# Optimization experiments

Measured on AMD Instinct MI355X. Metric: run time of the kernel, lower is better.

Reference implementation:

```python
import jax, jax.numpy as jnp
import numpy as np

N = 50000   # nodes
E = 800000  # edges
F_IN, H, C, G = 128, 96, 16, 128  # features, hidden, classes, graphs


def gelu(x):
    return jax.nn.gelu(x, approximate=False)  # torch F.gelu default (erf)


def gcn_conv(x, W, b, src, dst, dis):
    # PyG GCNConv improved=True: A_hat = A + 2I, out = D^-1/2 A_hat D^-1/2 (x W) + b
    xw = x @ W                                   # [N, out]
    norm = dis[src] * dis[dst]                   # [E]
    msg = norm[:, None] * xw[src]                # gather + scale
    out = jax.ops.segment_sum(msg, dst, num_segments=N)
    out = out + (2.0 * dis * dis)[:, None] * xw  # self-loop with weight 2
    return out + b


def setup_inputs() -> dict:
    key = jax.random.key(0)
    ks = jax.random.split(key, 12)
    x = jax.random.normal(ks[0], (N, F_IN), dtype=jnp.float32)
    edge_index = jax.random.randint(ks[1], (2, E), 0, N, dtype=jnp.int64)
    batch = jnp.sort(jax.random.randint(ks[2], (N,), 0, G, dtype=jnp.int64))
    s = lambda fan_in: 1.0 / np.sqrt(fan_in)
    W0 = jax.random.uniform(ks[3], (F_IN, H), jnp.float32, -s(F_IN), s(F_IN))
    b0 = jnp.zeros((H,), jnp.float32)
    W1 = jax.random.uniform(ks[4], (H, H), jnp.float32, -s(H), s(H))
    b1 = jnp.zeros((H,), jnp.float32)
    W2 = jax.random.uniform(ks[5], (H, H), jnp.float32, -s(H), s(H))
    b2 = jnp.zeros((H,), jnp.float32)
    Wc1 = jax.random.uniform(ks[6], (2 * H, H), jnp.float32, -s(2 * H), s(2 * H))
    bc1 = jax.random.uniform(ks[7], (H,), jnp.float32, -s(2 * H), s(2 * H))
    Wc2 = jax.random.uniform(ks[8], (H, C), jnp.float32, -s(H), s(H))
    bc2 = jax.random.uniform(ks[9], (C,), jnp.float32, -s(H), s(H))
    return {"x": x, "edge_index": edge_index, "batch": batch,
            "W0": W0, "b0": b0, "W1": W1, "b1": b1, "W2": W2, "b2": b2,
            "Wc1": Wc1, "bc1": bc1, "Wc2": Wc2, "bc2": bc2}


def reference(x, edge_index, batch, W0, b0, W1, b1, W2, b2, Wc1, bc1, Wc2, bc2):
    src, dst = edge_index[0], edge_index[1]
    # degrees including self-loop weight 2 (improved=True)
    deg = jax.ops.segment_sum(jnp.ones((E,), x.dtype), dst, num_segments=N) + 2.0
    dis = jax.lax.rsqrt(deg)
    # layer 0: GCNConv(F_IN -> H)
    h = gcn_conv(x, W0, b0, src, dst, dis)
    # residual GCNConv layers (dropout is identity at inference)
    h = h + gcn_conv(gelu(h), W1, b1, src, dst, dis)
    h = h + gcn_conv(gelu(h), W2, b2, src, dst, dis)
    h = gelu(h)
    # global mean + max pooling per graph
    cnt = jax.ops.segment_sum(jnp.ones((N,), h.dtype), batch, num_segments=G)
    mean_p = jax.ops.segment_sum(h, batch, num_segments=G) / cnt[:, None]
    max_p = jax.ops.segment_max(h, batch, num_segments=G)
    p = jnp.concatenate([mean_p, max_p], axis=1)  # [G, 2H]
    p = p @ Wc1 + bc1
    p = gelu(p)
    return p @ Wc2 + bc2
```

## Files before the change

### kernel.cpp

```cpp
#include <hip/hip_runtime.h>
#include <hip/hip_bf16.h>

#define DEVINL __device__ __forceinline__

constexpr int N = 50000;
constexpr int E = 800000;
constexpr int F_IN = 128;
constexpr int H = 96;
constexpr int C = 16;
constexpr int G = 128;
constexpr int S = 8;
constexpr int ELLW = 64;

constexpr int OFF_W0  = 0;
constexpr int OFF_W1  = OFF_W0 + F_IN * H;
constexpr int OFF_W2  = OFF_W1 + H * H;
constexpr int OFF_WC1 = OFF_W2 + H * H;
constexpr int OFF_WC2 = OFF_WC1 + 2 * H * H;
constexpr int OFF_B0  = OFF_WC2 + H * C;
constexpr int OFF_B1  = OFF_B0 + H;
constexpr int OFF_B2  = OFF_B1 + H;
constexpr int OFF_BC1 = OFF_B2 + H;
constexpr int OFF_BC2 = OFF_BC1 + H;
constexpr int WF_TOT  = OFF_BC2 + C;

constexpr int CVB   = (WF_TOT + 255) / 256;
constexpr int GEMB  = (N + 31) / 32;
constexpr int SCATB = (E / 2 + 127) / 128;

DEVINL float gelu_f(float x) {
    return 0.5f * x * (1.0f + erff(x * 0.70710678118654752440f));
}

DEVINL int detect_eidx_i64(const int* e) {
    int z = 0;
#pragma unroll
    for (int i = 1; i < 16; i += 2) z |= e[i];
    return z == 0;
}
DEVINL int detect_batch_i64(const int* a) {
    int z = 0;
    for (int i = 20001; i < 20032; i += 2) z |= a[i];
    return z == 0;
}
DEVINL int detect_x_f32(const unsigned short* xu) {
    int bad = 0;
    for (int i = 0; i < 128; i += 2) { int ex = (xu[i] >> 7) & 0xFF; if (ex >= 132) bad = 1; }
    return bad;
}

DEVINL unsigned pk(float a, float b) {
    __hip_bfloat16 ha = __float2bfloat16(a), hb = __float2bfloat16(b);
    unsigned short ua = *(unsigned short*)&ha, ub = *(unsigned short*)&hb;
    return (unsigned)ua | ((unsigned)ub << 16);
}
DEVINL float lo16(unsigned u) { return __uint_as_float(u << 16); }
DEVINL float hi16(unsigned u) { return __uint_as_float(u & 0xffff0000u); }

DEVINL float disv(int c) { return rsqrtf((float)c + 2.0f); }

__global__ void k_prep(const void* W0, const void* W1, const void* W2,
                       const void* Wc1, const void* Wc2,
                       const void* b0, const void* b1, const void* b2,
                       const void* bc1, const void* bc2,
                       const void* x, float* __restrict__ wf, int* __restrict__ cnt) {
    int i = blockIdx.x * 256 + threadIdx.x;
    if (i < N) cnt[i] = 0;
    if (i >= WF_TOT) return;
    int f32 = detect_x_f32((const unsigned short*)x);
    const void* src; int j;
    if      (i < OFF_W1)  { src = W0;  j = i - OFF_W0; }
    else if (i < OFF_W2)  { src = W1;  j = i - OFF_W1; }
    else if (i < OFF_WC1) { src = W2;  j = i - OFF_W2; }
    else if (i < OFF_WC2) { src = Wc1; j = i - OFF_WC1; }
    else if (i < OFF_B0)  { src = Wc2; j = i - OFF_WC2; }
    else if (i < OFF_B1)  { src = b0;  j = i - OFF_B0; }
    else if (i < OFF_B2)  { src = b1;  j = i - OFF_B1; }
    else if (i < OFF_BC1) { src = b2;  j = i - OFF_B2; }
    else if (i < OFF_BC2) { src = bc1; j = i - OFF_BC1; }
    else                  { src = bc2; j = i - OFF_BC2; }
    wf[i] = f32 ? ((const float*)src)[j]
                : __bfloat162float(((const __hip_bfloat16*)src)[j]);
}

template<int K, int KC, bool RAW_IN, bool GELU_IN, bool SCALE_OUT>
DEVINL void gemm_tile(const void* __restrict__ inp, const float* __restrict__ Wf,
                      const int* __restrict__ cnt,
                      int xf32, unsigned* __restrict__ out, int bid, int t) {
    constexpr int R = 32;
    constexpr int NC = K / KC;
    __shared__ __align__(16) float xs[KC][R + 4];
    __shared__ __align__(16) float wsh[KC * 96];
    const int r0 = bid * R;
    const int ty = t >> 4;
    const int tx = t & 15;

    float acc[4][6];
#pragma unroll
    for (int i = 0; i < 4; ++i)
#pragma unroll
        for (int j = 0; j < 6; ++j) acc[i][j] = 0.f;

    for (int c = 0; c < NC; ++c) {
        if (c) __syncthreads();
        for (int idx = t * 4; idx < KC * 96; idx += 128 * 4)
            *(float4*)&wsh[idx] = *(const float4*)&Wf[c * KC * 96 + idx];
        if (RAW_IN && !xf32) {
            for (int idx = t; idx < R * KC; idx += 128) {
                int r = idx / KC, kk = idx - r * KC;
                int row = r0 + r, k = c * KC + kk;
                float v = 0.f;
                if (row < N) v = __bfloat162float(((const __hip_bfloat16*)inp)[(size_t)row * K + k]);
                xs[kk][r] = v;
            }
        } else {
            constexpr int KC4 = KC / 4;
            for (int idx = t; idx < R * KC4; idx += 128) {
                int r = idx / KC4, k4 = (idx - r * KC4) * 4;
                int row = r0 + r, k = c * KC + k4;
                float4 v = make_float4(0.f, 0.f, 0.f, 0.f);
                if (row < N) v = *(const float4*)((const float*)inp + (size_t)row * K + k);
                if (GELU_IN) { v.x = gelu_f(v.x); v.y = gelu_f(v.y); v.z = gelu_f(v.z); v.w = gelu_f(v.w); }
                xs[k4 + 0][r] = v.x; xs[k4 + 1][r] = v.y; xs[k4 + 2][r] = v.z; xs[k4 + 3][r] = v.w;
            }
        }
        __syncthreads();

#pragma unroll 4
        for (int kk = 0; kk < KC; ++kk) {
            float4 av = *(const float4*)&xs[kk][ty * 4];
            float2 b0 = *(const float2*)&wsh[kk * 96 + tx * 6];
            float2 b1 = *(const float2*)&wsh[kk * 96 + tx * 6 + 2];
            float2 b2 = *(const float2*)&wsh[kk * 96 + tx * 6 + 4];
            float a[4] = {av.x, av.y, av.z, av.w};
            float b[6] = {b0.x, b0.y, b1.x, b1.y, b2.x, b2.y};
#pragma unroll
            for (int i = 0; i < 4; ++i)
#pragma unroll
                for (int j = 0; j < 6; ++j)
                    acc[i][j] = fmaf(a[i], b[j], acc[i][j]);
        }
    }

#pragma unroll
    for (int i = 0; i < 4; ++i) {
        int row = r0 + ty * 4 + i;
        if (row < N) {
            float d = SCALE_OUT ? disv(cnt[row]) : 1.0f;
            unsigned* o = out + (size_t)row * 48 + tx * 3;
            o[0] = pk(d * acc[i][0], d * acc[i][1]);
            o[1] = pk(d * acc[i][2], d * acc[i][3]);
            o[2] = pk(d * acc[i][4], d * acc[i][5]);
        }
    }
}

__global__ __launch_bounds__(128) void k_sg(const void* __restrict__ x,
                                            const float* __restrict__ Wf,
                                            const int* __restrict__ eidx,
                                            int* __restrict__ cnt, int* __restrict__ ell,
                                            unsigned* __restrict__ outZ) {
    int b = blockIdx.x, t = threadIdx.x;
    if (b % 3 == 0) {
        int gb = b / 3;
        if (gb >= GEMB) return;
        int xf32 = detect_x_f32((const unsigned short*)x);
        gemm_tile<F_IN, 32, true, false, false>(x, Wf, nullptr, xf32, outZ, gb, t);
        return;
    }
    int sb = (b / 3) * 2 + (b % 3) - 1;
    if (sb >= SCATB) return;
    int t2 = sb * 128 + t;
    int e = 2 * t2;
    if (e >= E) return;
    int i64 = detect_eidx_i64(eidx);
    int s0, s1, d0, d1;
    if (i64) {
        int4 sp = *(const int4*)(eidx + 4 * t2);
        int4 dp = *(const int4*)(eidx + 2 * E + 4 * t2);
        s0 = sp.x; s1 = sp.z; d0 = dp.x; d1 = dp.z;
    } else {
        int2 sp = *(const int2*)(eidx + 2 * t2);
        int2 dp = *(const int2*)(eidx + E + 2 * t2);
        s0 = sp.x; s1 = sp.y; d0 = dp.x; d1 = dp.y;
    }
    int p0 = atomicAdd(&cnt[d0], 1);
    if (p0 < ELLW) ell[d0 * ELLW + p0] = s0;
    if (e + 1 < E) {
        int p1 = atomicAdd(&cnt[d1], 1);
        if (p1 < ELLW) ell[d1 * ELLW + p1] = s1;
    }
}

template<int K, int KC, bool GELU_IN>
__global__ __launch_bounds__(128) void k_gemm(const float* __restrict__ inp,
                                              const float* __restrict__ Wf,
                                              const int* __restrict__ cnt,
                                              unsigned* __restrict__ out) {
    gemm_tile<K, KC, false, GELU_IN, true>(inp, Wf, cnt, 1, out, blockIdx.x, threadIdx.x);
}

template<bool PRESCALED>
__global__ __launch_bounds__(256) void k_aggr(const unsigned* __restrict__ xw, const float* res,
                                              const int* __restrict__ ell, const int* __restrict__ cnt,
                                              const float* __restrict__ bias, float* __restrict__ out) {
    __shared__ int   sIdx[4][ELLW];
    __shared__ float sW[4][ELLW];
    int wid = threadIdx.x >> 6, lane = threadIdx.x & 63;
    int n = blockIdx.x * 4 + wid;
    if (n >= N) return;
    int cn = cnt[n];
    int cc = min(cn, ELLW);
    if (lane < cc) {
        int idx = ell[n * ELLW + lane];
        sIdx[wid][lane] = idx;
        if (!PRESCALED) sW[wid][lane] = disv(cnt[idx]);
    }
    int slot = lane / 12;
    int li = lane - slot * 12;
    int cp = li * 4;

    int   idxs[5];
    float ws[5];
#pragma unroll
    for (int s = 0; s < 5; ++s) {
        int js = slot + 5 * s;
        bool valid = (slot < 5) && (js < cc);
        int raw = sIdx[wid][js & (ELLW - 1)];
        float rw = PRESCALED ? 1.f : sW[wid][js & (ELLW - 1)];
        idxs[s] = valid ? raw : n;
        ws[s]   = valid ? rw : 0.f;
    }
    uint4 u0 = *(const uint4*)(xw + (size_t)idxs[0] * 48 + cp);
    uint4 u1 = *(const uint4*)(xw + (size_t)idxs[1] * 48 + cp);
    uint4 u2 = *(const uint4*)(xw + (size_t)idxs[2] * 48 + cp);
    uint4 u3 = *(const uint4*)(xw + (size_t)idxs[3] * 48 + cp);
    uint4 u4 = *(const uint4*)(xw + (size_t)idxs[4] * 48 + cp);

    float4 A0 = make_float4(0.f, 0.f, 0.f, 0.f);
    float4 A1 = make_float4(0.f, 0.f, 0.f, 0.f);
#define ACCW(W_, U_) \
    A0.x = fmaf(W_, lo16((U_).x), A0.x); A0.y = fmaf(W_, hi16((U_).x), A0.y); \
    A0.z = fmaf(W_, lo16((U_).y), A0.z); A0.w = fmaf(W_, hi16((U_).y), A0.w); \
    A1.x = fmaf(W_, lo16((U_).z), A1.x); A1.y = fmaf(W_, hi16((U_).z), A1.y); \
    A1.z = fmaf(W_, lo16((U_).w), A1.z); A1.w = fmaf(W_, hi16((U_).w), A1.w);
    ACCW(ws[0], u0)
    ACCW(ws[1], u1)
    ACCW(ws[2], u2)
    ACCW(ws[3], u3)
    ACCW(ws[4], u4)

    int jt = (slot < 5) ? (25 + slot) : cc;
    for (; jt < cc; jt += 5) {
        int sdx = sIdx[wid][jt];
        uint4 u = *(const uint4*)(xw + (size_t)sdx * 48 + cp);
        float wt = PRESCALED ? 1.f : sW[wid][jt];
        ACCW(wt, u)
    }
#undef ACCW

    {
        float g0, g1, g2, g3;
        g0 = __shfl(A0.x, lane + 12); g1 = __shfl(A0.x, lane + 24); g2 = __shfl(A0.x, lane + 36); g3 = __shfl(A0.x, lane + 48);
        A0.x += g0 + g1 + g2 + g3;
        g0 = __shfl(A0.y, lane + 12); g1 = __shfl(A0.y, lane + 24); g2 = __shfl(A0.y, lane + 36); g3 = __shfl(A0.y, lane + 48);
        A0.y += g0 + g1 + g2 + g3;
        g0 = __shfl(A0.z, lane + 12); g1 = __shfl(A0.z, lane + 24); g2 = __shfl(A0.z, lane + 36); g3 = __shfl(A0.z, lane + 48);
        A0.z += g0 + g1 + g2 + g3;
        g0 = __shfl(A0.w, lane + 12); g1 = __shfl(A0.w, lane + 24); g2 = __shfl(A0.w, lane + 36); g3 = __shfl(A0.w, lane + 48);
        A0.w += g0 + g1 + g2 + g3;
        g0 = __shfl(A1.x, lane + 12); g1 = __shfl(A1.x, lane + 24); g2 = __shfl(A1.x, lane + 36); g3 = __shfl(A1.x, lane + 48);
        A1.x += g0 + g1 + g2 + g3;
        g0 = __shfl(A1.y, lane + 12); g1 = __shfl(A1.y, lane + 24); g2 = __shfl(A1.y, lane + 36); g3 = __shfl(A1.y, lane + 48);
        A1.y += g0 + g1 + g2 + g3;
        g0 = __shfl(A1.z, lane + 12); g1 = __shfl(A1.z, lane + 24); g2 = __shfl(A1.z, lane + 36); g3 = __shfl(A1.z, lane + 48);
        A1.z += g0 + g1 + g2 + g3;
        g0 = __shfl(A1.w, lane + 12); g1 = __shfl(A1.w, lane + 24); g2 = __shfl(A1.w, lane + 36); g3 = __shfl(A1.w, lane + 48);
        A1.w += g0 + g1 + g2 + g3;
    }

    if (lane < 12) {
        float dn = disv(cn);
        float sc = PRESCALED ? (2.f * dn) : (2.f * dn * dn);
        int cl = li * 8;
        uint4 su = *(const uint4*)(xw + (size_t)n * 48 + cp);
        float4 sv0 = make_float4(lo16(su.x), hi16(su.x), lo16(su.y), hi16(su.y));
        float4 sv1 = make_float4(lo16(su.z), hi16(su.z), lo16(su.w), hi16(su.w));
        float4 bv0 = *(const float4*)(bias + cl);
        float4 bv1 = *(const float4*)(bias + cl + 4);
        float4 rv0 = make_float4(0.f, 0.f, 0.f, 0.f);
        float4 rv1 = make_float4(0.f, 0.f, 0.f, 0.f);
        if (res) {
            rv0 = *(const float4*)(res + (size_t)n * 96 + cl);
            rv1 = *(const float4*)(res + (size_t)n * 96 + cl + 4);
        }
        float4 o0, o1;
        o0.x = rv0.x + dn * A0.x + sc * sv0.x + bv0.x;
        o0.y = rv0.y + dn * A0.y + sc * sv0.y + bv0.y;
        o0.z = rv0.z + dn * A0.z + sc * sv0.z + bv0.z;
        o0.w = rv0.w + dn * A0.w + sc * sv0.w + bv0.w;
        o1.x = rv1.x + dn * A1.x + sc * sv1.x + bv1.x;
        o1.y = rv1.y + dn * A1.y + sc * sv1.y + bv1.y;
        o1.z = rv1.z + dn * A1.z + sc * sv1.z + bv1.z;
        o1.w = rv1.w + dn * A1.w + sc * sv1.w + bv1.w;
        *(float4*)(out + (size_t)n * 96 + cl) = o0;
        *(float4*)(out + (size_t)n * 96 + cl + 4) = o1;
    }
}

DEVINL int ld_idx(const int* a, int i64, int i) { return i64 ? a[2 * i] : a[i]; }

DEVINL int lbound_s(const int* a, int i64, int n, int key) {
    int lo = 0, hi = n;
    while (lo < hi) { int m = (lo + hi) >> 1; if (ld_idx(a, i64, m) < key) lo = m + 1; else hi = m; }
    return lo;
}

__global__ __launch_bounds__(128) void k_pool(const float* __restrict__ h, const int* __restrict__ batch,
                                              float* __restrict__ part) {
    int i64 = detect_batch_i64(batch);
    int g = blockIdx.x / S, sch = blockIdx.x % S;
    int lo = lbound_s(batch, i64, N, g), hi = lbound_s(batch, i64, N, g + 1);
    int len = hi - lo;
    int a = lo + (int)(((long long)len * sch) / S);
    int b = lo + (int)(((long long)len * (sch + 1)) / S);
    int t = threadIdx.x;
    if (t < 96) {
        float s0 = 0.f, s1 = 0.f, m0 = -INFINITY, m1 = -INFINITY;
        int n = a;
        for (; n + 1 < b; n += 2) {
            float v0 = gelu_f(h[(size_t)n * 96 + t]);
            float v1 = gelu_f(h[(size_t)(n + 1) * 96 + t]);
            s0 += v0; s1 += v1;
            m0 = fmaxf(m0, v0); m1 = fmaxf(m1, v1);
        }
        if (n < b) {
            float v = gelu_f(h[(size_t)n * 96 + t]);
            s0 += v; m0 = fmaxf(m0, v);
        }
        part[(size_t)blockIdx.x * 192 + t] = s0 + s1;
        part[(size_t)blockIdx.x * 192 + 96 + t] = fmaxf(m0, m1);
    }
}

__global__ __launch_bounds__(128) void k_cls(const float* __restrict__ part, const int* __restrict__ batch,
                                             const void* __restrict__ x,
                                             const float* __restrict__ wf, void* __restrict__ outp) {
    __shared__ float p[192];
    __shared__ float q[96];
    int i64 = detect_batch_i64(batch);
    int g = blockIdx.x, t = threadIdx.x;
    int lo = lbound_s(batch, i64, N, g), hi = lbound_s(batch, i64, N, g + 1);
    float inv = (hi > lo) ? 1.f / (float)(hi - lo) : 0.f;
    if (t < 96) {
        float sum = 0.f, mx = -INFINITY;
        for (int s = 0; s < S; ++s) {
            sum += part[(size_t)(g * S + s) * 192 + t];
            mx = fmaxf(mx, part[(size_t)(g * S + s) * 192 + 96 + t]);
        }
        p[t] = sum * inv;
        p[96 + t] = mx;
    }
    __syncthreads();
    if (t < 96) {
        float acc = wf[OFF_BC1 + t];
        const float* Wc1 = wf + OFF_WC1;
        for (int j = 0; j < 192; ++j)
            acc += p[j] * Wc1[j * 96 + t];
        q[t] = gelu_f(acc);
    }
    __syncthreads();
    if (t < 16) {
        float acc = wf[OFF_BC2 + t];
        const float* Wc2 = wf + OFF_WC2;
        for (int j = 0; j < 96; ++j)
            acc += q[j] * Wc2[j * 16 + t];
        if (detect_x_f32((const unsigned short*)x)) ((float*)outp)[g * 16 + t] = acc;
        else ((__hip_bfloat16*)outp)[g * 16 + t] = __float2bfloat16(acc);
    }
}

extern "C" void kernel_launch(void* const* d_in, const int* in_sizes, int n_in,
                              void* d_out, int out_size, void* d_ws, size_t ws_size,
                              hipStream_t stream) {
    const void* x    = d_in[0];
    const int* eidx  = (const int*)d_in[1];
    const int* batch = (const int*)d_in[2];
    (void)in_sizes; (void)n_in; (void)out_size; (void)ws_size;

    char* w = (char*)d_ws;
    size_t off = 0;
    auto take = [&](size_t bytes) { size_t o = off; off += (bytes + 511) & ~(size_t)511; return o; };
    int*      cnt  = (int*)     (w + take((size_t)N * 4));
    float*    wf   = (float*)   (w + take((size_t)WF_TOT * 4));
    int*      ell  = (int*)     (w + take((size_t)N * ELLW * 4));
    unsigned* bufA = (unsigned*)(w + take((size_t)N * 48 * 4));
    float*    bufH = (float*)   (w + take((size_t)N * 96 * 4));
    float*    part = (float*)   (w + take((size_t)G * S * 192 * 4));

    k_prep<<<CVB, 256, 0, stream>>>(d_in[3], d_in[5], d_in[7], d_in[9], d_in[11],
                                    d_in[4], d_in[6], d_in[8], d_in[10], d_in[12],
                                    x, wf, cnt);
    k_sg<<<3 * GEMB, 128, 0, stream>>>(x, wf + OFF_W0, eidx, cnt, ell, bufA);

    int aggr_grid = (N + 3) / 4;
    k_aggr<false><<<aggr_grid, 256, 0, stream>>>(bufA, nullptr, ell, cnt, wf + OFF_B0, bufH);
    k_gemm<H, 48, true><<<GEMB, 128, 0, stream>>>(bufH, wf + OFF_W1, cnt, bufA);
    k_aggr<true><<<aggr_grid, 256, 0, stream>>>(bufA, bufH, ell, cnt, wf + OFF_B1, bufH);
    k_gemm<H, 48, true><<<GEMB, 128, 0, stream>>>(bufH, wf + OFF_W2, cnt, bufA);
    k_aggr<true><<<aggr_grid, 256, 0, stream>>>(bufA, bufH, ell, cnt, wf + OFF_B2, bufH);

    k_pool<<<G * S, 128, 0, stream>>>(bufH, batch, part);
    k_cls<<<G, 128, 0, stream>>>(part, batch, x, wf, d_out);
}
```

Before: 350.3 us.

## Split bf16 XW buffer into two column halves and aggregate each half separately

The packed bf16 XW matrix is now stored as two separate 48-column arrays, one per feature half. The aggregation grid doubles so each block gathers only one half, letting a wave cover 10 neighbours per pass with 6 lanes each instead of 5 with 12. Each half array is smaller, which should improve cache locality for random neighbour gathers. In exchange, neighbour index and count loads are repeated for every node, and the cross-lane reduction gains an extra shuffle step.

New measurement: 417.8 us. +19.3%, slower.

```diff
diff --git a/kernel.cpp b/kernel.cpp
--- a/kernel.cpp
+++ b/kernel.cpp
@@ -27,6 +27,7 @@
 constexpr int CVB   = (WF_TOT + 255) / 256;
 constexpr int GEMB  = (N + 31) / 32;
 constexpr int SCATB = (E / 2 + 127) / 128;
+constexpr int AGGRB = (N + 3) / 4;
 
 DEVINL float gelu_f(float x) {
     return 0.5f * x * (1.0f + erff(x * 0.70710678118654752440f));
@@ -86,7 +87,8 @@
 template<int K, int KC, bool RAW_IN, bool GELU_IN, bool SCALE_OUT>
 DEVINL void gemm_tile(const void* __restrict__ inp, const float* __restrict__ Wf,
                       const int* __restrict__ cnt,
-                      int xf32, unsigned* __restrict__ out, int bid, int t) {
+                      int xf32, unsigned* __restrict__ outLo, unsigned* __restrict__ outHi,
+                      int bid, int t) {
     constexpr int R = 32;
     constexpr int NC = K / KC;
     __shared__ __align__(16) float xs[KC][R + 4];
@@ -147,7 +149,8 @@
         int row = r0 + ty * 4 + i;
         if (row < N) {
             float d = SCALE_OUT ? disv(cnt[row]) : 1.0f;
-            unsigned* o = out + (size_t)row * 48 + tx * 3;
+            unsigned* o = (tx < 8) ? (outLo + (size_t)row * 24 + tx * 3)
+                                   : (outHi + (size_t)row * 24 + (tx - 8) * 3);
             o[0] = pk(d * acc[i][0], d * acc[i][1]);
             o[1] = pk(d * acc[i][2], d * acc[i][3]);
             o[2] = pk(d * acc[i][4], d * acc[i][5]);
@@ -159,13 +162,14 @@
                                             const float* __restrict__ Wf,
                                             const int* __restrict__ eidx,
                                             int* __restrict__ cnt, int* __restrict__ ell,
-                                            unsigned* __restrict__ outZ) {
+                                            unsigned* __restrict__ outLo,
+                                            unsigned* __restrict__ outHi) {
     int b = blockIdx.x, t = threadIdx.x;
     if (b % 3 == 0) {
         int gb = b / 3;
         if (gb >= GEMB) return;
         int xf32 = detect_x_f32((const unsigned short*)x);
-        gemm_tile<F_IN, 32, true, false, false>(x, Wf, nullptr, xf32, outZ, gb, t);
+        gemm_tile<F_IN, 32, true, false, false>(x, Wf, nullptr, xf32, outLo, outHi, gb, t);
         return;
     }
     int sb = (b / 3) * 2 + (b % 3) - 1;
@@ -196,19 +200,25 @@
 __global__ __launch_bounds__(128) void k_gemm(const float* __restrict__ inp,
                                               const float* __restrict__ Wf,
                                               const int* __restrict__ cnt,
-                                              unsigned* __restrict__ out) {
-    gemm_tile<K, KC, false, GELU_IN, true>(inp, Wf, cnt, 1, out, blockIdx.x, threadIdx.x);
+                                              unsigned* __restrict__ outLo,
+                                              unsigned* __restrict__ outHi) {
+    gemm_tile<K, KC, false, GELU_IN, true>(inp, Wf, cnt, 1, outLo, outHi, blockIdx.x, threadIdx.x);
 }
 
 template<bool PRESCALED>
-__global__ __launch_bounds__(256) void k_aggr(const unsigned* __restrict__ xw, const float* res,
+__global__ __launch_bounds__(256) void k_aggr(const unsigned* __restrict__ xwLo,
+                                              const unsigned* __restrict__ xwHi,
+                                              const float* res,
                                               const int* __restrict__ ell, const int* __restrict__ cnt,
                                               const float* __restrict__ bias, float* __restrict__ out) {
     __shared__ int   sIdx[4][ELLW];
     __shared__ float sW[4][ELLW];
     int wid = threadIdx.x >> 6, lane = threadIdx.x & 63;
-    int n = blockIdx.x * 4 + wid;
+    int half = (blockIdx.x >= AGGRB) ? 1 : 0;
+    int nb = blockIdx.x - half * AGGRB;
+    int n = nb * 4 + wid;
     if (n >= N) return;
+    const unsigned* xw = half ? xwHi : xwLo;
     int cn = cnt[n];
     int cc = min(cn, ELLW);
     if (lane < cc) {
@@ -216,26 +226,24 @@
         sIdx[wid][lane] = idx;
         if (!PRESCALED) sW[wid][lane] = disv(cnt[idx]);
     }
-    int slot = lane / 12;
-    int li = lane - slot * 12;
+    int slot = lane / 6;
+    int li = lane - slot * 6;
     int cp = li * 4;
 
-    int   idxs[5];
-    float ws[5];
-#pragma unroll
-    for (int s = 0; s < 5; ++s) {
-        int js = slot + 5 * s;
-        bool valid = (slot < 5) && (js < cc);
+    int   idxs[3];
+    float ws[3];
+#pragma unroll
+    for (int s = 0; s < 3; ++s) {
+        int js = slot + 10 * s;
+        bool valid = (slot < 10) && (js < cc);
         int raw = sIdx[wid][js & (ELLW - 1)];
         float rw = PRESCALED ? 1.f : sW[wid][js & (ELLW - 1)];
         idxs[s] = valid ? raw : n;
         ws[s]   = valid ? rw : 0.f;
     }
-    uint4 u0 = *(const uint4*)(xw + (size_t)idxs[0] * 48 + cp);
-    uint4 u1 = *(const uint4*)(xw + (size_t)idxs[1] * 48 + cp);
-    uint4 u2 = *(const uint4*)(xw + (size_t)idxs[2] * 48 + cp);
-    uint4 u3 = *(const uint4*)(xw + (size_t)idxs[3] * 48 + cp);
-    uint4 u4 = *(const uint4*)(xw + (size_t)idxs[4] * 48 + cp);
+    uint4 u0 = *(const uint4*)(xw + (size_t)idxs[0] * 24 + cp);
+    uint4 u1 = *(const uint4*)(xw + (size_t)idxs[1] * 24 + cp);
+    uint4 u2 = *(const uint4*)(xw + (size_t)idxs[2] * 24 + cp);
 
     float4 A0 = make_float4(0.f, 0.f, 0.f, 0.f);
     float4 A1 = make_float4(0.f, 0.f, 0.f, 0.f);
@@ -247,52 +255,59 @@
     ACCW(ws[0], u0)
     ACCW(ws[1], u1)
     ACCW(ws[2], u2)
-    ACCW(ws[3], u3)
-    ACCW(ws[4], u4)
-
-    int jt = (slot < 5) ? (25 + slot) : cc;
-    for (; jt < cc; jt += 5) {
+
+    int jt = (slot < 10) ? (30 + slot) : cc;
+    for (; jt < cc; jt += 10) {
         int sdx = sIdx[wid][jt];
-        uint4 u = *(const uint4*)(xw + (size_t)sdx * 48 + cp);
+        uint4 u = *(const uint4*)(xw + (size_t)sdx * 24 + cp);
         float wt = PRESCALED ? 1.f : sW[wid][jt];
         ACCW(wt, u)
     }
 #undef ACCW
 
     {
+        float g;
+        g = __shfl(A0.x, lane + 30); A0.x += g;
+        g = __shfl(A0.y, lane + 30); A0.y += g;
+        g = __shfl(A0.z, lane + 30); A0.z += g;
+        g = __shfl(A0.w, lane + 30); A0.w += g;
+        g = __shfl(A1.x, lane + 30); A1.x += g;
+        g = __shfl(A1.y, lane + 30); A1.y += g;
+        g = __shfl(A1.z, lane + 30); A1.z += g;
+        g = __shfl(A1.w, lane + 30); A1.w += g;
         float g0, g1, g2, g3;
-        g0 = __shfl(A0.x, lane + 12); g1 = __shfl(A0.x, lane + 24); g2 = __shfl(A0.x, lane + 36); g3 = __shfl(A0.x, lane + 48);
+        g0 = __shfl(A0.x, lane + 6); g1 = __shfl(A0.x, lane + 12); g2 = __shfl(A0.x, lane + 18); g3 = __shfl(A0.x, lane + 24);
         A0.x += g0 + g1 + g2 + g3;
-        g0 = __shfl(A0.y, lane + 12); g1 = __shfl(A0.y, lane + 24); g2 = __shfl(A0.y, lane + 36); g3 = __shfl(A0.y, lane + 48);
+        g0 = __shfl(A0.y, lane + 6); g1 = __shfl(A0.y, lane + 12); g2 = __shfl(A0.y, lane + 18); g3 = __shfl(A0.y, lane + 24);
         A0.y += g0 + g1 + g2 + g3;
-        g0 = __shfl(A0.z, lane + 12); g1 = __shfl(A0.z, lane + 24); g2 = __shfl(A0.z, lane + 36); g3 = __shfl(A0.z, lane + 48);
+        g0 = __shfl(A0.z, lane + 6); g1 = __shfl(A0.z, lane + 12); g2 = __shfl(A0.z, lane + 18); g3 = __shfl(A0.z, lane + 24);
         A0.z += g0 + g1 + g2 + g3;
-        g0 = __shfl(A0.w, lane + 12); g1 = __shfl(A0.w, lane + 24); g2 = __shfl(A0.w, lane + 36); g3 = __shfl(A0.w, lane + 48);
+        g0 = __shfl(A0.w, lane + 6); g1 = __shfl(A0.w, lane + 12); g2 = __shfl(A0.w, lane + 18); g3 = __shfl(A0.w, lane + 24);
         A0.w += g0 + g1 + g2 + g3;
-        g0 = __shfl(A1.x, lane + 12); g1 = __shfl(A1.x, lane + 24); g2 = __shfl(A1.x, lane + 36); g3 = __shfl(A1.x, lane + 48);
+        g0 = __shfl(A1.x, lane + 6); g1 = __shfl(A1.x, lane + 12); g2 = __shfl(A1.x, lane + 18); g3 = __shfl(A1.x, lane + 24);
         A1.x += g0 + g1 + g2 + g3;
-        g0 = __shfl(A1.y, lane + 12); g1 = __shfl(A1.y, lane + 24); g2 = __shfl(A1.y, lane + 36); g3 = __shfl(A1.y, lane + 48);
+        g0 = __shfl(A1.y, lane + 6); g1 = __shfl(A1.y, lane + 12); g2 = __shfl(A1.y, lane + 18); g3 = __shfl(A1.y, lane + 24);
         A1.y += g0 + g1 + g2 + g3;
-        g0 = __shfl(A1.z, lane + 12); g1 = __shfl(A1.z, lane + 24); g2 = __shfl(A1.z, lane + 36); g3 = __shfl(A1.z, lane + 48);
+        g0 = __shfl(A1.z, lane + 6); g1 = __shfl(A1.z, lane + 12); g2 = __shfl(A1.z, lane + 18); g3 = __shfl(A1.z, lane + 24);
         A1.z += g0 + g1 + g2 + g3;
-        g0 = __shfl(A1.w, lane + 12); g1 = __shfl(A1.w, lane + 24); g2 = __shfl(A1.w, lane + 36); g3 = __shfl(A1.w, lane + 48);
+        g0 = __shfl(A1.w, lane + 6); g1 = __shfl(A1.w, lane + 12); g2 = __shfl(A1.w, lane + 18); g3 = __shfl(A1.w, lane + 24);
         A1.w += g0 + g1 + g2 + g3;
     }
 
-    if (lane < 12) {
+    if (lane < 6) {
         float dn = disv(cn);
         float sc = PRESCALED ? (2.f * dn) : (2.f * dn * dn);
-        int cl = li * 8;
-        uint4 su = *(const uint4*)(xw + (size_t)n * 48 + cp);
+        int gcol = half * 48 + li * 8;
+        uint4 su = *(const uint4*)(xw + (size_t)n * 24 + cp);
         float4 sv0 = make_float4(lo16(su.x), hi16(su.x), lo16(su.y), hi16(su.y));
         float4 sv1 = make_float4(lo16(su.z), hi16(su.z), lo16(su.w), hi16(su.w));
-        float4 bv0 = *(const float4*)(bias + cl);
-        float4 bv1 = *(const float4*)(bias + cl + 4);
+        float4 bv0 = *(const float4*)(bias + gcol);
+        float4 bv1 = *(const float4*)(bias + gcol + 4);
         float4 rv0 = make_float4(0.f, 0.f, 0.f, 0.f);
         float4 rv1 = make_float4(0.f, 0.f, 0.f, 0.f);
         if (res) {
-            rv0 = *(const float4*)(res + (size_t)n * 96 + cl);
-            rv1 = *(const float4*)(res + (size_t)n * 96 + cl + 4);
+            rv0 = *(const float4*)(res + (size_t)n * 96 + gcol);
+            rv1 = *(const float4*)(res + (size_t)n * 96 + gcol + 4);
         }
         float4 o0, o1;
         o0.x = rv0.x + dn * A0.x + sc * sv0.x + bv0.x;
@@ -303,8 +318,8 @@
         o1.y = rv1.y + dn * A1.y + sc * sv1.y + bv1.y;
         o1.z = rv1.z + dn * A1.z + sc * sv1.z + bv1.z;
         o1.w = rv1.w + dn * A1.w + sc * sv1.w + bv1.w;
-        *(float4*)(out + (size_t)n * 96 + cl) = o0;
-        *(float4*)(out + (size_t)n * 96 + cl + 4) = o1;
+        *(float4*)(out + (size_t)n * 96 + gcol) = o0;
+        *(float4*)(out + (size_t)n * 96 + gcol + 4) = o1;
     }
 }
 
@@ -391,24 +406,24 @@
     char* w = (char*)d_ws;
     size_t off = 0;
     auto take = [&](size_t bytes) { size_t o = off; off += (bytes + 511) & ~(size_t)511; return o; };
-    int*      cnt  = (int*)     (w + take((size_t)N * 4));
-    float*    wf   = (float*)   (w + take((size_t)WF_TOT * 4));
-    int*      ell  = (int*)     (w + take((size_t)N * ELLW * 4));
-    unsigned* bufA = (unsigned*)(w + take((size_t)N * 48 * 4));
-    float*    bufH = (float*)   (w + take((size_t)N * 96 * 4));
-    float*    part = (float*)   (w + take((size_t)G * S * 192 * 4));
+    int*      cnt    = (int*)     (w + take((size_t)N * 4));
+    float*    wf     = (float*)   (w + take((size_t)WF_TOT * 4));
+    int*      ell    = (int*)     (w + take((size_t)N * ELLW * 4));
+    unsigned* bufAlo = (unsigned*)(w + take((size_t)N * 24 * 4));
+    unsigned* bufAhi = (unsigned*)(w + take((size_t)N * 24 * 4));
+    float*    bufH   = (float*)   (w + take((size_t)N * 96 * 4));
+    float*    part   = (float*)   (w + take((size_t)G * S * 192 * 4));
 
     k_prep<<<CVB, 256, 0, stream>>>(d_in[3], d_in[5], d_in[7], d_in[9], d_in[11],
                                     d_in[4], d_in[6], d_in[8], d_in[10], d_in[12],
                                     x, wf, cnt);
-    k_sg<<<3 * GEMB, 128, 0, stream>>>(x, wf + OFF_W0, eidx, cnt, ell, bufA);
-
-    int aggr_grid = (N + 3) / 4;
-    k_aggr<false><<<aggr_grid, 256, 0, stream>>>(bufA, nullptr, ell, cnt, wf + OFF_B0, bufH);
-    k_gemm<H, 48, true><<<GEMB, 128, 0, stream>>>(bufH, wf + OFF_W1, cnt, bufA);
-    k_aggr<true><<<aggr_grid, 256, 0, stream>>>(bufA, bufH, ell, cnt, wf + OFF_B1, bufH);
-    k_gemm<H, 48, true><<<GEMB, 128, 0, stream>>>(bufH, wf + OFF_W2, cnt, bufA);
-    k_aggr<true><<<aggr_grid, 256, 0, stream>>>(bufA, bufH, ell, cnt, wf + OFF_B2, bufH);
+    k_sg<<<3 * GEMB, 128, 0, stream>>>(x, wf + OFF_W0, eidx, cnt, ell, bufAlo, bufAhi);
+
+    k_aggr<false><<<2 * AGGRB, 256, 0, stream>>>(bufAlo, bufAhi, nullptr, ell, cnt, wf + OFF_B0, bufH);
+    k_gemm<H, 48, true><<<GEMB, 128, 0, stream>>>(bufH, wf + OFF_W1, cnt, bufAlo, bufAhi);
+    k_aggr<true><<<2 * AGGRB, 256, 0, stream>>>(bufAlo, bufAhi, bufH, ell, cnt, wf + OFF_B1, bufH);
+    k_gemm<H, 48, true><<<GEMB, 128, 0, stream>>>(bufH, wf + OFF_W2, cnt, bufAlo, bufAhi);
+    k_aggr<true><<<2 * AGGRB, 256, 0, stream>>>(bufAlo, bufAhi, bufH, ell, cnt, wf + OFF_B2, bufH);
 
     k_pool<<<G * S, 128, 0, stream>>>(bufH, batch, part);
     k_cls<<<G, 128, 0, stream>>>(part, batch, x, wf, d_out);
```

## Use bf16 MFMA with split hi/lo weights for hidden-layer GEMMs

Applied to the files above, without the earlier changes.

Replaces the scalar FP32 GEMM for the two hidden GCN layers with a matrix-core kernel that uses 16x16x32 bf16 MFMA instructions. The activations get GELU applied and are cast to bf16. Each weight matrix is split in the prep kernel into a bf16 high part and a bf16 low residual, both prepacked into the MFMA operand layout, so weight precision is kept near FP32. The aim is to move GEMM arithmetic onto the matrix cores. The cost is bf16 rounding of the activations and an extra prep pass.

Result: faster. 314.2 us (-10.3%).

```diff
diff --git a/kernel.cpp b/kernel.cpp
--- a/kernel.cpp
+++ b/kernel.cpp
@@ -25,8 +25,12 @@
 constexpr int WF_TOT  = OFF_BC2 + C;
 
 constexpr int CVB   = (WF_TOT + 255) / 256;
+constexpr int FRB   = (2 * H * H + 255) / 256;
 constexpr int GEMB  = (N + 31) / 32;
 constexpr int SCATB = (E / 2 + 127) / 128;
+
+using short8 = __attribute__((ext_vector_type(8))) short;
+using f32x4  = __attribute__((ext_vector_type(4))) float;
 
 DEVINL float gelu_f(float x) {
     return 0.5f * x * (1.0f + erff(x * 0.70710678118654752440f));
@@ -56,6 +60,11 @@
 }
 DEVINL float lo16(unsigned u) { return __uint_as_float(u << 16); }
 DEVINL float hi16(unsigned u) { return __uint_as_float(u & 0xffff0000u); }
+DEVINL unsigned short bfb(float f) {
+    __hip_bfloat16 h = __float2bfloat16(f);
+    return *(unsigned short*)&h;
+}
+DEVINL float bf2f(unsigned short u) { return __uint_as_float((unsigned)u << 16); }
 
 DEVINL float disv(int c) { return rsqrtf((float)c + 2.0f); }
 
@@ -63,8 +72,31 @@
                        const void* Wc1, const void* Wc2,
                        const void* b0, const void* b1, const void* b2,
                        const void* bc1, const void* bc2,
-                       const void* x, float* __restrict__ wf, int* __restrict__ cnt) {
-    int i = blockIdx.x * 256 + threadIdx.x;
+                       const void* x, float* __restrict__ wf, int* __restrict__ cnt,
+                       unsigned short* __restrict__ wfr) {
+    int b = blockIdx.x, t = threadIdx.x;
+    if (b >= CVB) {
+        int f = (b - CVB) * 256 + t;
+        if (f >= 2 * H * H) return;
+        int layer = f / (H * H);
+        int e = f - layer * H * H;
+        int k = e / 96, n = e - k * 96;
+        const void* src = layer ? W2 : W1;
+        int f32 = detect_x_f32((const unsigned short*)x);
+        float wv = f32 ? ((const float*)src)[e]
+                       : __bfloat162float(((const __hip_bfloat16*)src)[e]);
+        unsigned short hi = bfb(wv);
+        unsigned short lo = bfb(wv - bf2f(hi));
+        int kt = k >> 5, kk = k & 31;
+        int lane = (kk >> 3) * 16 + (n & 15);
+        int nt = n >> 4, i = kk & 7;
+        int pos = ((kt * 6 + nt) * 64 + lane) * 8 + i;
+        unsigned short* base = wfr + (size_t)layer * 2 * H * H;
+        base[pos] = hi;
+        base[H * H + pos] = lo;
+        return;
+    }
+    int i = b * 256 + t;
     if (i < N) cnt[i] = 0;
     if (i >= WF_TOT) return;
     int f32 = detect_x_f32((const unsigned short*)x);
@@ -192,12 +224,61 @@
     }
 }
 
-template<int K, int KC, bool GELU_IN>
-__global__ __launch_bounds__(128) void k_gemm(const float* __restrict__ inp,
-                                              const float* __restrict__ Wf,
-                                              const int* __restrict__ cnt,
-                                              unsigned* __restrict__ out) {
-    gemm_tile<K, KC, false, GELU_IN, true>(inp, Wf, cnt, 1, out, blockIdx.x, threadIdx.x);
+__global__ __launch_bounds__(128) void k_mgemm(const float* __restrict__ inp,
+                                               const unsigned short* __restrict__ wfr,
+                                               const int* __restrict__ cnt,
+                                               unsigned* __restrict__ out) {
+    int t = threadIdx.x;
+    int wv = t >> 6, lane = t & 63;
+    int r0 = blockIdx.x * 32 + wv * 16;
+    int arow = r0 + (lane & 15);
+    int kc = (lane >> 4) * 8;
+
+    f32x4 acc[6];
+#pragma unroll
+    for (int i = 0; i < 6; ++i) acc[i] = (f32x4){0.f, 0.f, 0.f, 0.f};
+
+#pragma unroll
+    for (int kt = 0; kt < 3; ++kt) {
+        float a[8];
+        if (arow < N) {
+            float4 v0 = *(const float4*)(inp + (size_t)arow * 96 + kt * 32 + kc);
+            float4 v1 = *(const float4*)(inp + (size_t)arow * 96 + kt * 32 + kc + 4);
+            a[0] = v0.x; a[1] = v0.y; a[2] = v0.z; a[3] = v0.w;
+            a[4] = v1.x; a[5] = v1.y; a[6] = v1.z; a[7] = v1.w;
+        } else {
+#pragma unroll
+            for (int i = 0; i < 8; ++i) a[i] = 0.f;
+        }
+        short8 af;
+#pragma unroll
+        for (int i = 0; i < 8; ++i) af[i] = (short)bfb(gelu_f(a[i]));
+#pragma unroll
+        for (int nt = 0; nt < 6; ++nt) {
+            const unsigned short* bp = wfr + ((kt * 6 + nt) * 64 + lane) * 8;
+            short8 bh = *(const short8*)bp;
+            short8 bl = *(const short8*)(bp + H * H);
+            acc[nt] = __builtin_amdgcn_mfma_f32_16x16x32_bf16(af, bh, acc[nt], 0, 0, 0);
+            acc[nt] = __builtin_amdgcn_mfma_f32_16x16x32_bf16(af, bl, acc[nt], 0, 0, 0);
+        }
+    }
+
+    int rbase = r0 + (lane >> 4) * 4;
+    float d[4];
+#pragma unroll
+    for (int j = 0; j < 4; ++j)
+        d[j] = (rbase + j < N) ? disv(cnt[rbase + j]) : 0.f;
+#pragma unroll
+    for (int nt = 0; nt < 6; ++nt) {
+        int c = nt * 16 + (lane & 15);
+#pragma unroll
+        for (int j = 0; j < 4; ++j) {
+            float v = acc[nt][j] * d[j];
+            float p = __shfl_xor(v, 1);
+            if (!(lane & 1) && rbase + j < N)
+                out[(size_t)(rbase + j) * 48 + (c >> 1)] = pk(v, p);
+        }
+    }
 }
 
 template<bool PRESCALED>
@@ -391,23 +472,24 @@
     char* w = (char*)d_ws;
     size_t off = 0;
     auto take = [&](size_t bytes) { size_t o = off; off += (bytes + 511) & ~(size_t)511; return o; };
-    int*      cnt  = (int*)     (w + take((size_t)N * 4));
-    float*    wf   = (float*)   (w + take((size_t)WF_TOT * 4));
-    int*      ell  = (int*)     (w + take((size_t)N * ELLW * 4));
-    unsigned* bufA = (unsigned*)(w + take((size_t)N * 48 * 4));
-    float*    bufH = (float*)   (w + take((size_t)N * 96 * 4));
-    float*    part = (float*)   (w + take((size_t)G * S * 192 * 4));
-
-    k_prep<<<CVB, 256, 0, stream>>>(d_in[3], d_in[5], d_in[7], d_in[9], d_in[11],
-                                    d_in[4], d_in[6], d_in[8], d_in[10], d_in[12],
-                                    x, wf, cnt);
+    int*            cnt  = (int*)           (w + take((size_t)N * 4));
+    float*          wf   = (float*)         (w + take((size_t)WF_TOT * 4));
+    int*            ell  = (int*)           (w + take((size_t)N * ELLW * 4));
+    unsigned*       bufA = (unsigned*)      (w + take((size_t)N * 48 * 4));
+    float*          bufH = (float*)         (w + take((size_t)N * 96 * 4));
+    float*          part = (float*)         (w + take((size_t)G * S * 192 * 4));
+    unsigned short* wfr  = (unsigned short*)(w + take((size_t)4 * H * H * 2));
+
+    k_prep<<<CVB + FRB, 256, 0, stream>>>(d_in[3], d_in[5], d_in[7], d_in[9], d_in[11],
+                                          d_in[4], d_in[6], d_in[8], d_in[10], d_in[12],
+                                          x, wf, cnt, wfr);
     k_sg<<<3 * GEMB, 128, 0, stream>>>(x, wf + OFF_W0, eidx, cnt, ell, bufA);
 
     int aggr_grid = (N + 3) / 4;
     k_aggr<false><<<aggr_grid, 256, 0, stream>>>(bufA, nullptr, ell, cnt, wf + OFF_B0, bufH);
-    k_gemm<H, 48, true><<<GEMB, 128, 0, stream>>>(bufH, wf + OFF_W1, cnt, bufA);
+    k_mgemm<<<GEMB, 128, 0, stream>>>(bufH, wfr, cnt, bufA);
     k_aggr<true><<<aggr_grid, 256, 0, stream>>>(bufA, bufH, ell, cnt, wf + OFF_B1, bufH);
-    k_gemm<H, 48, true><<<GEMB, 128, 0, stream>>>(bufH, wf + OFF_W2, cnt, bufA);
+    k_mgemm<<<GEMB, 128, 0, stream>>>(bufH, wfr + 2 * H * H, cnt, bufA);
     k_aggr<true><<<aggr_grid, 256, 0, stream>>>(bufA, bufH, ell, cnt, wf + OFF_B2, bufH);
 
     k_pool<<<G * S, 128, 0, stream>>>(bufH, batch, part);
```
